# Kernel optimization log

Measured on AMD Instinct MI355X. Metric: run time of the kernel, lower is better.

Reference implementation:

```python
import jax, jax.numpy as jnp
import numpy as np

B, N, H, A, S = 8, 8192, 256, 64, 32  # batch, nodes, hidden, annotation, sub_graphs


def _mysoftmax(x):
    # exp, zero out where x <= 0, normalize over last dim, nan (0/0) -> 0
    x_exp = jnp.where(x > 0, jnp.exp(x), 0.0)
    part = jnp.sum(x_exp, axis=-1, keepdims=True)
    # safe divide: where partition == 0 the faithful result after nan_to_num is 0
    return jnp.where(part > 0, x_exp / jnp.where(part > 0, part, 1.0), 0.0)


def setup_inputs() -> dict:
    key = jax.random.key(0)
    k1, k2, k3, k4, k5, k6 = jax.random.split(key, 6)
    x = jax.random.normal(k1, (B, N, H + A), dtype=jnp.float32)
    node_map = jax.random.uniform(k2, (B, S, N), dtype=jnp.float32)
    lim = 1.0 / np.sqrt(H + A)
    Wi = jax.random.uniform(k3, (H, H + A), minval=-lim, maxval=lim, dtype=jnp.float32)
    bi = jax.random.uniform(k4, (H,), minval=-lim, maxval=lim, dtype=jnp.float32)
    Wj = jax.random.uniform(k5, (H, H + A), minval=-lim, maxval=lim, dtype=jnp.float32)
    bj = jax.random.uniform(k6, (H,), minval=-lim, maxval=lim, dtype=jnp.float32)
    return {"x": x, "node_map": node_map, "Wi": Wi, "bi": bi, "Wj": Wj, "bj": bj}


def reference(x, node_map, Wi, bi, Wj, bj):
    # gated node features: sigmoid(fc_i(x)) * tanh(fc_j(x))  -> [B, N, H]
    x_sigm = jax.nn.sigmoid(jnp.einsum('bnf,hf->bnh', x, Wi) + bi)
    x_tanh = jnp.tanh(jnp.einsum('bnf,hf->bnh', x, Wj) + bj)
    x_all = x_sigm * x_tanh
    # per-node L2 norm -> [B, 1, N]
    x_norm = jnp.linalg.norm(x_all, axis=-1)[:, None, :]
    # scaled subgraph map and masked softmax over nodes -> [B, S, N]
    weight = _mysoftmax(node_map * x_norm)
    # weighted sum over nodes (replaces [B,S,N,H] broadcast) -> [B, S, H]
    pooled = jnp.einsum('bsn,bnh->bsh', weight, x_all)
    return jnp.tanh(pooled), weight[..., None]
```

## Files before the change

kernel.cpp:

```cpp
#include <hip/hip_runtime.h>
#include <cstdint>
#include <cstddef>

typedef unsigned short u16;
typedef unsigned int   u32;
using short8 = __attribute__((ext_vector_type(8))) short;
using f32x4  = __attribute__((ext_vector_type(4))) float;

#define NB    8
#define NN    8192
#define HH    256
#define FF    320
#define SS    32
#define NROWS 65536
#define NCH   32

__device__ __forceinline__ u16 f2bf(float f) {
    union { float f; u32 u; } v; v.f = f;
    u32 r = v.u + 0x7fffu + ((v.u >> 16) & 1u);
    return (u16)(r >> 16);
}
__device__ __forceinline__ u32 pk2(float lo, float hi) {
    u32 r;
    asm("v_cvt_pk_bf16_f32 %0, %1, %2" : "=v"(r) : "v"(lo), "v"(hi));
    return r;
}

__global__ __launch_bounds__(256) void prep_all(
    const float* __restrict__ x, const float* __restrict__ Wi,
    const float* __restrict__ Wj,
    u16* __restrict__ xb16, u16* __restrict__ Wb, float* __restrict__ normsq)
{
    int gid = blockIdx.x * 256 + threadIdx.x;
    #pragma unroll
    for (int i = 0; i < 5; ++i) {
        size_t o = (size_t)gid + (size_t)i * 524288;
        const float4* s = reinterpret_cast<const float4*>(x + o * 8);
        float4 a = s[0], b = s[1];
        union { u32 u[4]; uint4 v; } r;
        r.u[0] = pk2(a.x, a.y); r.u[1] = pk2(a.z, a.w);
        r.u[2] = pk2(b.x, b.y); r.u[3] = pk2(b.z, b.w);
        *reinterpret_cast<uint4*>(xb16 + o * 8) = r.v;
    }
    if (gid < 163840) {
        float v = (gid < 81920) ? Wi[gid] : Wj[gid - 81920];
        Wb[gid] = f2bf(v);
    }
    if (gid < NROWS) normsq[gid] = 0.f;
}

__global__ __launch_bounds__(512, 4) void gemm_gate(
    const u16* __restrict__ xb16, const u16* __restrict__ Wb,
    const float* __restrict__ bi, const float* __restrict__ bj,
    u16* __restrict__ xa, float* __restrict__ normsq)
{
    __shared__ u16 lB[5 * 8192];

    const int bx   = blockIdx.x;
    const int xcd  = bx & 7;
    const int ht   = (bx >> 3) & 3;
    const int slot = bx >> 5;
    const int mb   = xcd + slot * 8;
    const int m0   = mb * 256;
    const int h0   = ht * 64;
    const int b_idx = m0 >> 13;
    const int n0    = m0 & 8191;

    const int tid  = threadIdx.x;
    const int w    = tid >> 6;
    const int lane = tid & 63;
    const int quad = lane >> 4;
    const int l15  = lane & 15;

    {
        const int rsub = lane >> 3;
        const int kg   = (lane & 7) ^ rsub;
        #pragma unroll
        for (int kt = 0; kt < 5; ++kt) {
            #pragma unroll
            for (int j = 0; j < 2; ++j) {
                int sl  = w * 2 + j;
                int row = sl * 8 + rsub;
                int mat = row >> 6, hl = row & 63;
                const u16* gsrc = Wb + mat * 81920 + (size_t)(h0 + hl) * FF + kt * 64 + kg * 8;
                u16* ldst = &lB[kt * 8192 + sl * 512];
                __builtin_amdgcn_global_load_lds(
                    (const __attribute__((address_space(1))) void*)gsrc,
                    (__attribute__((address_space(3))) void*)ldst, 16, 0, 0);
            }
        }
    }

    const u16* xb = xb16 + (size_t)(m0 + w * 32 + l15) * FF + quad * 8;

    f32x4 acc[8][2];
    #pragma unroll
    for (int a = 0; a < 8; ++a)
        #pragma unroll
        for (int m = 0; m < 2; ++m) acc[a][m] = (f32x4){0.f, 0.f, 0.f, 0.f};

    short8 pre[4][2];
    #pragma unroll
    for (int p = 0; p < 3; ++p)
        #pragma unroll
        for (int mt = 0; mt < 2; ++mt)
            pre[p][mt] = *reinterpret_cast<const short8*>(xb + mt * 16 * FF + p * 32);

    __syncthreads();

    #pragma unroll
    for (int ks = 0; ks < 10; ++ks) {
        const int cur = ks & 3;
        if (ks < 7) {
            const int nxt = (ks + 3) & 3;
            const int f   = (ks + 3) * 32;
            #pragma unroll
            for (int mt = 0; mt < 2; ++mt)
                pre[nxt][mt] = *reinterpret_cast<const short8*>(xb + mt * 16 * FF + f);
        }
        const int kt = ks >> 1, kk = ks & 1;
        #pragma unroll
        for (int mn = 0; mn < 8; ++mn) {
            int c = mn * 16 + l15;
            short8 bv = *reinterpret_cast<const short8*>(
                &lB[kt * 8192 + c * 64 + (((kk * 4 + quad) ^ (c & 7)) << 3)]);
            acc[mn][0] = __builtin_amdgcn_mfma_f32_16x16x32_bf16(pre[cur][0], bv, acc[mn][0], 0, 0, 0);
            acc[mn][1] = __builtin_amdgcn_mfma_f32_16x16x32_bf16(pre[cur][1], bv, acc[mn][1], 0, 0, 0);
        }
    }

    float s0[2][4];
    #pragma unroll
    for (int mt = 0; mt < 2; ++mt)
        #pragma unroll
        for (int r = 0; r < 4; ++r) s0[mt][r] = 0.f;

    #pragma unroll
    for (int hq = 0; hq < 4; ++hq) {
        int h = h0 + hq * 16 + l15;
        float bi_v = bi[h], bj_v = bj[h];
        #pragma unroll
        for (int mt = 0; mt < 2; ++mt) {
            float xall[4];
            #pragma unroll
            for (int r = 0; r < 4; ++r) {
                float yi = acc[hq][mt][r] + bi_v;
                float yj = acc[hq + 4][mt][r] + bj_v;
                float sg = 1.f / (1.f + __expf(-yi));
                float e2 = __expf(-2.f * yj);
                float th = (1.f - e2) / (1.f + e2);
                float xv = sg * th;
                xall[r] = xv;
                s0[mt][r] += xv * xv;
            }
            uint2 pk;
            pk.x = pk2(xall[0], xall[1]);
            pk.y = pk2(xall[2], xall[3]);
            size_t o = (size_t)b_idx * ((size_t)HH * NN) + (size_t)h * NN
                     + (size_t)(n0 + w * 32 + mt * 16 + quad * 4);
            *reinterpret_cast<uint2*>(&xa[o]) = pk;
        }
    }
    #pragma unroll
    for (int m = 1; m <= 8; m <<= 1) {
        #pragma unroll
        for (int mt = 0; mt < 2; ++mt)
            #pragma unroll
            for (int r = 0; r < 4; ++r)
                s0[mt][r] += __shfl_xor(s0[mt][r], m, 64);
    }
    if (l15 == 0) {
        #pragma unroll
        for (int mt = 0; mt < 2; ++mt)
            #pragma unroll
            for (int r = 0; r < 4; ++r)
                atomicAdd(&normsq[m0 + w * 32 + mt * 16 + quad * 4 + r], s0[mt][r]);
    }
}

__global__ __launch_bounds__(1024) void softmax_k(
    const float* __restrict__ nm, const float* __restrict__ normsq,
    float* __restrict__ out1)
{
    __shared__ float red[16];
    int bs = blockIdx.x;
    int b  = bs >> 5;
    const float* src = nm + (size_t)bs * NN;
    float* dst       = out1 + (size_t)bs * NN;
    const float* ns  = normsq + (size_t)b * NN;
    int tid = threadIdx.x;
    float e[8];
    float sum = 0.f;
    #pragma unroll
    for (int i = 0; i < 8; ++i) {
        int n = i * 1024 + tid;
        float logit = src[n] * sqrtf(ns[n]);
        float v = (logit > 0.f) ? __expf(logit) : 0.f;
        e[i] = v;
        sum += v;
    }
    #pragma unroll
    for (int m = 1; m <= 32; m <<= 1) sum += __shfl_xor(sum, m, 64);
    int w = tid >> 6, lane = tid & 63;
    if (lane == 0) red[w] = sum;
    __syncthreads();
    float part = 0.f;
    #pragma unroll
    for (int j = 0; j < 16; ++j) part += red[j];
    float inv = (part > 0.f) ? (1.f / part) : 0.f;
    #pragma unroll
    for (int i = 0; i < 8; ++i) dst[i * 1024 + tid] = e[i] * inv;
}

__global__ __launch_bounds__(256) void pooled_k(
    const u16* __restrict__ xa, const float* __restrict__ wgt,
    float* __restrict__ part)
{
    __shared__ u16 lw[32 * 264];
    int bx = blockIdx.x;
    int ht = bx >> 8;
    int bc = bx & 255;
    int b  = bc >> 5, c = bc & 31;
    int n0 = c * 256;
    int tid = threadIdx.x, w = tid >> 6, lane = tid & 63, quad = lane >> 4, l15 = lane & 15;

    {
        int s  = tid >> 3;
        int nb = (tid & 7) * 32;
        const float* src = wgt + (size_t)(b * SS + s) * NN + n0 + nb;
        #pragma unroll
        for (int q = 0; q < 8; ++q) {
            float4 v = *reinterpret_cast<const float4*>(src + q * 4);
            uint2 pk;
            pk.x = pk2(v.x, v.y);
            pk.y = pk2(v.z, v.w);
            *reinterpret_cast<uint2*>(&lw[s * 264 + nb + q * 4]) = pk;
        }
    }
    __syncthreads();

    f32x4 acc[2];
    acc[0] = (f32x4){0.f, 0.f, 0.f, 0.f};
    acc[1] = (f32x4){0.f, 0.f, 0.f, 0.f};

    const u16* ab = xa + (size_t)b * ((size_t)HH * NN)
                  + (size_t)(ht * 64 + w * 16 + l15) * NN + n0;
    #pragma unroll
    for (int ks = 0; ks < 8; ++ks) {
        short8 av = *reinterpret_cast<const short8*>(ab + ks * 32 + quad * 8);
        #pragma unroll
        for (int st = 0; st < 2; ++st) {
            int s = st * 16 + l15;
            short8 bv = *reinterpret_cast<const short8*>(&lw[s * 264 + ks * 32 + quad * 8]);
            acc[st] = __builtin_amdgcn_mfma_f32_16x16x32_bf16(av, bv, acc[st], 0, 0, 0);
        }
    }
    float* pb = part + (size_t)(b * NCH + c) * 8192;
    #pragma unroll
    for (int st = 0; st < 2; ++st) {
        int h = ht * 64 + w * 16 + quad * 4;
        int s = st * 16 + l15;
        *reinterpret_cast<f32x4*>(&pb[s * 256 + h]) = acc[st];
    }
}

__global__ __launch_bounds__(256) void reduce_tanh(const float* __restrict__ part,
                                                   float* __restrict__ out0)
{
    int gid = blockIdx.x * 256 + threadIdx.x;
    int b = gid >> 13, r = gid & 8191;
    const float* p = part + (size_t)b * NCH * 8192 + r;
    float s = 0.f;
    #pragma unroll
    for (int c = 0; c < NCH; ++c) s += p[(size_t)c * 8192];
    out0[gid] = tanhf(s);
}

extern "C" void kernel_launch(void* const* d_in, const int* in_sizes, int n_in,
                              void* d_out, int out_size, void* d_ws, size_t ws_size,
                              hipStream_t stream) {
    const float* x  = (const float*)d_in[0];
    const float* nm = (const float*)d_in[1];
    const float* Wi = (const float*)d_in[2];
    const float* bi = (const float*)d_in[3];
    const float* Wj = (const float*)d_in[4];
    const float* bj = (const float*)d_in[5];
    float* out0 = (float*)d_out;
    float* out1 = out0 + NB * SS * HH;

    char* ws = (char*)d_ws;
    u16*   Wb     = (u16*)ws;
    u16*   xb16   = (u16*)(ws + 327680);
    u16*   xa     = (u16*)(ws + 327680 + 41943040);
    float* normsq = (float*)(ws + 327680 + 41943040 + 33554432);
    float* part   = (float*)(ws + 327680 + 41943040 + 33554432 + 262144);

    prep_all   <<<2048, 256, 0, stream>>>(x, Wi, Wj, xb16, Wb, normsq);
    gemm_gate  <<<1024, 512, 0, stream>>>(xb16, Wb, bi, bj, xa, normsq);
    softmax_k  <<<256, 1024, 0, stream>>>(nm, normsq, out1);
    pooled_k   <<<1024, 256, 0, stream>>>(xa, out1, part);
    reduce_tanh<<<256,  256, 0, stream>>>(part, out0);
}
```

Measured before the change: 200.3 us.

## Process two M-tiles per gate GEMM block to reuse the staged weight tile

The gate GEMM kernel now handles two 256-row M tiles per block against the same LDS-resident weight slice, halving the grid from 1024 to 512 blocks. Weight staging into LDS is amortised over twice the work, and the first A-fragments of the second tile are prefetched before the first tile's epilogue runs, overlapping loads with the epilogue math. The cost is fewer blocks, which may leave the GPU less evenly loaded, and more serial work per block.

After: 217.9 us. 1.09x slower.

```diff
diff --git a/kernel.cpp b/kernel.cpp
--- a/kernel.cpp
+++ b/kernel.cpp
@@ -49,65 +49,14 @@
     if (gid < NROWS) normsq[gid] = 0.f;
 }
 
-__global__ __launch_bounds__(512, 4) void gemm_gate(
-    const u16* __restrict__ xb16, const u16* __restrict__ Wb,
-    const float* __restrict__ bi, const float* __restrict__ bj,
-    u16* __restrict__ xa, float* __restrict__ normsq)
-{
-    __shared__ u16 lB[5 * 8192];
-
-    const int bx   = blockIdx.x;
-    const int xcd  = bx & 7;
-    const int ht   = (bx >> 3) & 3;
-    const int slot = bx >> 5;
-    const int mb   = xcd + slot * 8;
-    const int m0   = mb * 256;
-    const int h0   = ht * 64;
-    const int b_idx = m0 >> 13;
-    const int n0    = m0 & 8191;
-
-    const int tid  = threadIdx.x;
-    const int w    = tid >> 6;
-    const int lane = tid & 63;
-    const int quad = lane >> 4;
-    const int l15  = lane & 15;
-
-    {
-        const int rsub = lane >> 3;
-        const int kg   = (lane & 7) ^ rsub;
-        #pragma unroll
-        for (int kt = 0; kt < 5; ++kt) {
-            #pragma unroll
-            for (int j = 0; j < 2; ++j) {
-                int sl  = w * 2 + j;
-                int row = sl * 8 + rsub;
-                int mat = row >> 6, hl = row & 63;
-                const u16* gsrc = Wb + mat * 81920 + (size_t)(h0 + hl) * FF + kt * 64 + kg * 8;
-                u16* ldst = &lB[kt * 8192 + sl * 512];
-                __builtin_amdgcn_global_load_lds(
-                    (const __attribute__((address_space(1))) void*)gsrc,
-                    (__attribute__((address_space(3))) void*)ldst, 16, 0, 0);
-            }
-        }
-    }
-
-    const u16* xb = xb16 + (size_t)(m0 + w * 32 + l15) * FF + quad * 8;
-
-    f32x4 acc[8][2];
-    #pragma unroll
-    for (int a = 0; a < 8; ++a)
-        #pragma unroll
-        for (int m = 0; m < 2; ++m) acc[a][m] = (f32x4){0.f, 0.f, 0.f, 0.f};
-
-    short8 pre[4][2];
-    #pragma unroll
-    for (int p = 0; p < 3; ++p)
-        #pragma unroll
-        for (int mt = 0; mt < 2; ++mt)
-            pre[p][mt] = *reinterpret_cast<const short8*>(xb + mt * 16 * FF + p * 32);
-
-    __syncthreads();
-
+__device__ __forceinline__ f32x4 mfma_bf16(short8 a, short8 b, f32x4 c) {
+    return __builtin_amdgcn_mfma_f32_16x16x32_bf16(a, b, c, 0, 0, 0);
+}
+
+__device__ __forceinline__ void gg_mainloop(
+    const u16* __restrict__ xb, const u16* lBp,
+    int l15, int quad, short8 (&pre)[4][2], f32x4 (&acc)[8][2])
+{
     #pragma unroll
     for (int ks = 0; ks < 10; ++ks) {
         const int cur = ks & 3;
@@ -123,12 +72,20 @@
         for (int mn = 0; mn < 8; ++mn) {
             int c = mn * 16 + l15;
             short8 bv = *reinterpret_cast<const short8*>(
-                &lB[kt * 8192 + c * 64 + (((kk * 4 + quad) ^ (c & 7)) << 3)]);
-            acc[mn][0] = __builtin_amdgcn_mfma_f32_16x16x32_bf16(pre[cur][0], bv, acc[mn][0], 0, 0, 0);
-            acc[mn][1] = __builtin_amdgcn_mfma_f32_16x16x32_bf16(pre[cur][1], bv, acc[mn][1], 0, 0, 0);
-        }
-    }
-
+                &lBp[kt * 8192 + c * 64 + (((kk * 4 + quad) ^ (c & 7)) << 3)]);
+            acc[mn][0] = mfma_bf16(pre[cur][0], bv, acc[mn][0]);
+            acc[mn][1] = mfma_bf16(pre[cur][1], bv, acc[mn][1]);
+        }
+    }
+}
+
+__device__ __forceinline__ void gg_epilogue(
+    f32x4 (&acc)[8][2], int m0, int h0, int w, int lane,
+    const float* __restrict__ bi, const float* __restrict__ bj,
+    u16* __restrict__ xa, float* __restrict__ normsq)
+{
+    const int quad = lane >> 4, l15 = lane & 15;
+    const int b_idx = m0 >> 13, n0 = m0 & 8191;
     float s0[2][4];
     #pragma unroll
     for (int mt = 0; mt < 2; ++mt)
@@ -178,6 +135,82 @@
     }
 }
 
+__global__ __launch_bounds__(512, 4) void gemm_gate(
+    const u16* __restrict__ xb16, const u16* __restrict__ Wb,
+    const float* __restrict__ bi, const float* __restrict__ bj,
+    u16* __restrict__ xa, float* __restrict__ normsq)
+{
+    __shared__ u16 lB[5 * 8192];
+
+    const int bx   = blockIdx.x;
+    const int xcd  = bx & 7;
+    const int ht   = (bx >> 3) & 3;
+    const int pr   = bx >> 5;
+    const int h0   = ht * 64;
+    const int m0a  = (xcd + pr * 8) * 256;
+    const int m0b  = (xcd + (pr + 16) * 8) * 256;
+
+    const int tid  = threadIdx.x;
+    const int w    = tid >> 6;
+    const int lane = tid & 63;
+    const int quad = lane >> 4;
+    const int l15  = lane & 15;
+
+    {
+        const int rsub = lane >> 3;
+        const int kg   = (lane & 7) ^ rsub;
+        #pragma unroll
+        for (int kt = 0; kt < 5; ++kt) {
+            #pragma unroll
+            for (int j = 0; j < 2; ++j) {
+                int sl  = w * 2 + j;
+                int row = sl * 8 + rsub;
+                int mat = row >> 6, hl = row & 63;
+                const u16* gsrc = Wb + mat * 81920 + (size_t)(h0 + hl) * FF + kt * 64 + kg * 8;
+                u16* ldst = &lB[kt * 8192 + sl * 512];
+                __builtin_amdgcn_global_load_lds(
+                    (const __attribute__((address_space(1))) void*)gsrc,
+                    (__attribute__((address_space(3))) void*)ldst, 16, 0, 0);
+            }
+        }
+    }
+
+    const u16* xba = xb16 + (size_t)(m0a + w * 32 + l15) * FF + quad * 8;
+    const u16* xbb = xb16 + (size_t)(m0b + w * 32 + l15) * FF + quad * 8;
+
+    f32x4 acc[8][2];
+    short8 pre[4][2];
+
+    #pragma unroll
+    for (int p = 0; p < 3; ++p)
+        #pragma unroll
+        for (int mt = 0; mt < 2; ++mt)
+            pre[p][mt] = *reinterpret_cast<const short8*>(xba + mt * 16 * FF + p * 32);
+
+    __syncthreads();
+
+    #pragma unroll
+    for (int a = 0; a < 8; ++a)
+        #pragma unroll
+        for (int m = 0; m < 2; ++m) acc[a][m] = (f32x4){0.f, 0.f, 0.f, 0.f};
+    gg_mainloop(xba, lB, l15, quad, pre, acc);
+
+    #pragma unroll
+    for (int p = 0; p < 3; ++p)
+        #pragma unroll
+        for (int mt = 0; mt < 2; ++mt)
+            pre[p][mt] = *reinterpret_cast<const short8*>(xbb + mt * 16 * FF + p * 32);
+
+    gg_epilogue(acc, m0a, h0, w, lane, bi, bj, xa, normsq);
+
+    #pragma unroll
+    for (int a = 0; a < 8; ++a)
+        #pragma unroll
+        for (int m = 0; m < 2; ++m) acc[a][m] = (f32x4){0.f, 0.f, 0.f, 0.f};
+    gg_mainloop(xbb, lB, l15, quad, pre, acc);
+    gg_epilogue(acc, m0b, h0, w, lane, bi, bj, xa, normsq);
+}
+
 __global__ __launch_bounds__(1024) void softmax_k(
     const float* __restrict__ nm, const float* __restrict__ normsq,
     float* __restrict__ out1)
@@ -296,7 +329,7 @@
     float* part   = (float*)(ws + 327680 + 41943040 + 33554432 + 262144);
 
     prep_all   <<<2048, 256, 0, stream>>>(x, Wi, Wj, xb16, Wb, normsq);
-    gemm_gate  <<<1024, 512, 0, stream>>>(xb16, Wb, bi, bj, xa, normsq);
+    gemm_gate  <<<512,  512, 0, stream>>>(xb16, Wb, bi, bj, xa, normsq);
     softmax_k  <<<256, 1024, 0, stream>>>(nm, normsq, out1);
     pooled_k   <<<1024, 256, 0, stream>>>(xa, out1, part);
     reduce_tanh<<<256,  256, 0, stream>>>(part, out0);
```
